# Performance work log

Hardware: AMD Instinct MI355X
Metric: run time of the kernel (lower is better)

## Reference

```python
import jax, jax.numpy as jnp
import numpy as np

B = 256        # number of graphs
NPG = 256      # nodes per graph
N = B * NPG    # total nodes
F = 128        # node feature dim
DEG = 16       # avg degree
E = N * DEG    # total edges
LAT = [32, 32, 32, 1]
D = sum(LAT)   # total_latent_dim = 97
K = 30         # sortpool k
C1, C2, KW2 = 16, 32, 5
DENSE = ((K - 2) // 2 + 1 - KW2 + 1) * C2  # 352
OUT = 2


def setup_inputs() -> dict:
    key = jax.random.key(0)
    ks = jax.random.split(key, 16)
    node_feat = jax.random.normal(ks[0], (N, F), jnp.float32)
    # edges constrained within each graph (block-diagonal adjacency)
    base = ((jnp.arange(E, dtype=jnp.int32) // (E // B)) * NPG).astype(jnp.int32)
    src = jax.random.randint(ks[1], (E,), 0, NPG, dtype=jnp.int32) + base
    dst = jax.random.randint(ks[2], (E,), 0, NPG, dtype=jnp.int32) + base
    degs = jnp.zeros((N,), jnp.int32).at[dst].add(1)  # in-degree per node
    s = 0.1
    dims = [F] + LAT
    inp = {"node_feat": node_feat, "src": src, "dst": dst, "degs": degs}
    for i in range(4):
        inp[f"W{i}"] = jax.random.normal(ks[3 + i], (dims[i], dims[i + 1]), jnp.float32) * s
        inp[f"b{i}"] = jnp.zeros((dims[i + 1],), jnp.float32)
    inp["conv1_w"] = jax.random.normal(ks[8], (C1, 1, D), jnp.float32) * s
    inp["conv1_b"] = jnp.zeros((C1,), jnp.float32)
    inp["conv2_w"] = jax.random.normal(ks[9], (C2, C1, KW2), jnp.float32) * s
    inp["conv2_b"] = jnp.zeros((C2,), jnp.float32)
    inp["out_w"] = jax.random.normal(ks[10], (DENSE, OUT), jnp.float32) * s
    inp["out_b"] = jnp.zeros((OUT,), jnp.float32)
    return inp


def reference(node_feat, W0, b0, W1, b1, W2, b2, W3, b3,
              conv1_w, conv1_b, conv2_w, conv2_b, out_w, out_b,
              src, dst, degs):
    n = node_feat.shape[0]
    deg1 = (degs.astype(node_feat.dtype) + 1.0)[:, None]  # node_degs = deg + 1
    h = node_feat
    feats = []
    for W, b in ((W0, b0), (W1, b1), (W2, b2), (W3, b3)):
        # gnn_spmm(n2n, h) + h : sparse adjacency matmul via segment add
        pooled = jnp.zeros((n, h.shape[1]), h.dtype).at[dst].add(h[src]) + h
        h = jnp.tanh((pooled @ W + b) / deg1)
        feats.append(h)
    Z = jnp.concatenate(feats, axis=1)          # [N, D]
    Zb = Z.reshape(B, NPG, D)                   # equal-sized graphs
    # sortpooling: top-k on last latent channel per graph, gather rows
    _, idx = jax.lax.top_k(Zb[:, :, -1], K)     # [B, K]
    sp = jnp.take_along_axis(Zb, idx[:, :, None], axis=1)  # [B, K, D]
    x = sp.reshape(B, 1, K * D)
    dn = ('NCH', 'OIH', 'NCH')
    x = jax.lax.conv_general_dilated(x, conv1_w, (D,), 'VALID', dimension_numbers=dn)
    x = jax.nn.relu(x + conv1_b[None, :, None])          # [B, C1, K]
    x = x.reshape(B, C1, K // 2, 2).max(axis=-1)         # maxpool1d(2,2) -> [B, C1, 15]
    x = jax.lax.conv_general_dilated(x, conv2_w, (1,), 'VALID', dimension_numbers=dn)
    x = jax.nn.relu(x + conv2_b[None, :, None])          # [B, C2, 11]
    to_dense = x.reshape(B, -1)                          # [B, 352]
    out = jax.nn.relu(to_dense @ out_w + out_b)
    return jax.nn.relu(out)  # original applies conv1d_activation twice at the end
```

## Files before the change

kernel.cpp:

```cpp
#include <hip/hip_runtime.h>

#define NPG  256
#define EPG  4096
#define FDIM 128
#define KTOP 30

__global__ __launch_bounds__(256, 1)
void dgcnn_fused(const float* __restrict__ node_feat,
                 const int* __restrict__ srcv, const int* __restrict__ dstv,
                 const int* __restrict__ degs,
                 const float* __restrict__ W0, const float* __restrict__ b0,
                 const float* __restrict__ W1, const float* __restrict__ b1,
                 const float* __restrict__ W2, const float* __restrict__ b2,
                 const float* __restrict__ W3, const float* __restrict__ b3,
                 const float* __restrict__ cw1, const float* __restrict__ cb1,
                 const float* __restrict__ cw2, const float* __restrict__ cb2,
                 const float* __restrict__ ow,  const float* __restrict__ ob,
                 float* __restrict__ outp)
{
    __shared__ float Ybuf[NPG * 33];
    __shared__ int   srclist[EPG];
    __shared__ int   offs[NPG];
    __shared__ int   cnt [NPG];
    __shared__ int   degl[NPG];
    __shared__ float invd[NPG];
    __shared__ float keys[NPG];
    __shared__ int   sel [KTOP + 2];

    const int g = blockIdx.x;
    const int t = threadIdx.x;

    int dn = degs[g * NPG + t];
    degl[t] = dn;
    cnt[t]  = 0;
    invd[t] = 1.0f / (float)(dn + 1);
    offs[t] = dn;
    __syncthreads();
    for (int s = 1; s < NPG; s <<= 1) {
        int v = (t >= s) ? offs[t - s] : 0;
        __syncthreads();
        offs[t] += v;
        __syncthreads();
    }
    int excl = offs[t] - dn;
    __syncthreads();
    offs[t] = excl;
    __syncthreads();
    {
        const int* sg = srcv + g * EPG;
        const int* dg = dstv + g * EPG;
        for (int i = 0; i < EPG / NPG; i++) {
            int e  = t + i * NPG;
            int ss = sg[e] & (NPG - 1);
            int dd = dg[e] & (NPG - 1);
            int p  = atomicAdd(&cnt[dd], 1);
            srclist[offs[dd] + p] = ss;
        }
    }

    float acc[32];
    #pragma unroll
    for (int c = 0; c < 32; c++) acc[c] = 0.f;
    {
        const float* nf = node_feat + (size_t)g * NPG * FDIM;
        for (int kc = 0; kc < 4; kc++) {
            __syncthreads();
            #pragma unroll
            for (int i = 0; i < 8; i++) {
                int Fi = t + i * 256;
                int n  = Fi >> 3, k4 = Fi & 7;
                const float4 v = *(const float4*)(nf + n * FDIM + kc * 32 + k4 * 4);
                float* p = &Ybuf[n * 33 + k4 * 4];
                p[0] = v.x; p[1] = v.y; p[2] = v.z; p[3] = v.w;
            }
            __syncthreads();
            #pragma unroll
            for (int k = 0; k < 32; k++) {
                float h = Ybuf[t * 33 + k];
                const float* wr = W0 + (kc * 32 + k) * 32;
                #pragma unroll
                for (int c = 0; c < 32; c++) acc[c] = fmaf(h, wr[c], acc[c]);
            }
        }
        __syncthreads();
        #pragma unroll
        for (int c = 0; c < 32; c++) Ybuf[t * 33 + c] = acc[c];
        __syncthreads();
    }

    float h1[32], h2[32], h3[32];
    const float iv = invd[t];
    const int   o  = offs[t];
    const int   d  = degl[t];

    auto agg = [&](float (&h)[32]) {
        #pragma unroll
        for (int c = 0; c < 32; c++) h[c] = Ybuf[t * 33 + c];
        for (int j = 0; j < d; j++) {
            int a = srclist[o + j];
            const float* yr = &Ybuf[a * 33];
            #pragma unroll
            for (int c = 0; c < 32; c++) h[c] += yr[c];
        }
    };
    auto act = [&](float (&h)[32], const float* bb) {
        #pragma unroll
        for (int c = 0; c < 32; c++) h[c] = tanhf((h[c] + bb[c]) * iv);
    };
    auto matml = [&](const float (&h)[32], const float* Wn) {
        float a[32];
        #pragma unroll
        for (int c = 0; c < 32; c++) a[c] = 0.f;
        #pragma unroll
        for (int k = 0; k < 32; k++) {
            const float* wr = Wn + k * 32;
            float hk = h[k];
            #pragma unroll
            for (int c = 0; c < 32; c++) a[c] = fmaf(hk, wr[c], a[c]);
        }
        __syncthreads();
        #pragma unroll
        for (int c = 0; c < 32; c++) Ybuf[t * 33 + c] = a[c];
        __syncthreads();
    };

    agg(h1); act(h1, b0); matml(h1, W1);
    agg(h2); act(h2, b1); matml(h2, W2);
    agg(h3); act(h3, b2);
    {
        float a3 = 0.f;
        #pragma unroll
        for (int k = 0; k < 32; k++) a3 = fmaf(h3[k], W3[k], a3);
        __syncthreads();
        Ybuf[t * 33] = a3;
        __syncthreads();
    }
    float kv;
    {
        float s = Ybuf[t * 33];
        for (int j = 0; j < d; j++) s += Ybuf[srclist[o + j] * 33];
        kv = tanhf((s + b3[0]) * iv);
        keys[t] = kv;
    }
    __syncthreads();

    int rank = 0;
    #pragma unroll 4
    for (int j = 0; j < NPG; j++) {
        float vj = keys[j];
        rank += ((vj > kv) || ((vj == kv) && (j < t))) ? 1 : 0;
    }
    if (rank < KTOP) sel[rank] = t;
    __syncthreads();

    float* sp    = (float*)srclist;
    float* x1    = sp + 30 * 97;
    float* xp    = x1 + 480;
    float* dense = xp + 240;

    if (rank < KTOP) {
        float* dp = sp + rank * 97;
        #pragma unroll
        for (int c = 0; c < 32; c++) dp[c]      = h1[c];
        #pragma unroll
        for (int c = 0; c < 32; c++) dp[32 + c] = h2[c];
        #pragma unroll
        for (int c = 0; c < 32; c++) dp[64 + c] = h3[c];
        dp[96] = kv;
    }
    __syncthreads();

    for (int idx = t; idx < 480; idx += 256) {
        int k = idx >> 4, c = idx & 15;
        float s = cb1[c];
        for (int dd = 0; dd < 97; dd++) s = fmaf(sp[k * 97 + dd], cw1[c * 97 + dd], s);
        x1[c * 30 + k] = fmaxf(s, 0.f);
    }
    __syncthreads();
    for (int idx = t; idx < 240; idx += 256) {
        int c = idx / 15, k = idx - c * 15;
        xp[idx] = fmaxf(x1[c * 30 + 2 * k], x1[c * 30 + 2 * k + 1]);
    }
    __syncthreads();
    for (int idx = t; idx < 352; idx += 256) {
        int c = idx / 11, j = idx - c * 11;
        float s = cb2[c];
        for (int i2 = 0; i2 < 16; i2++) {
            #pragma unroll
            for (int tt = 0; tt < 5; tt++)
                s = fmaf(xp[i2 * 15 + j + tt], cw2[(c * 16 + i2) * 5 + tt], s);
        }
        dense[idx] = fmaxf(s, 0.f);
    }
    __syncthreads();
    if (t < 64) {
        float a0 = 0.f, a1 = 0.f;
        for (int dd = t; dd < 352; dd += 64) {
            float v = dense[dd];
            a0 = fmaf(v, ow[dd * 2],     a0);
            a1 = fmaf(v, ow[dd * 2 + 1], a1);
        }
        #pragma unroll
        for (int off2 = 32; off2 > 0; off2 >>= 1) {
            a0 += __shfl_down(a0, off2);
            a1 += __shfl_down(a1, off2);
        }
        if (t == 0) {
            outp[g * 2 + 0] = fmaxf(a0 + ob[0], 0.f);
            outp[g * 2 + 1] = fmaxf(a1 + ob[1], 0.f);
        }
    }
}

extern "C" void kernel_launch(void* const* d_in, const int* in_sizes, int n_in,
                              void* d_out, int out_size, void* d_ws, size_t ws_size,
                              hipStream_t stream) {
    const float* node_feat = (const float*)d_in[0];
    const int*   src       = (const int*)  d_in[1];
    const int*   dst       = (const int*)  d_in[2];
    const int*   degsp     = (const int*)  d_in[3];
    const float* W0 = (const float*)d_in[4];
    const float* b0 = (const float*)d_in[5];
    const float* W1 = (const float*)d_in[6];
    const float* b1 = (const float*)d_in[7];
    const float* W2 = (const float*)d_in[8];
    const float* b2 = (const float*)d_in[9];
    const float* W3 = (const float*)d_in[10];
    const float* b3 = (const float*)d_in[11];
    const float* cw1 = (const float*)d_in[12];
    const float* cb1 = (const float*)d_in[13];
    const float* cw2 = (const float*)d_in[14];
    const float* cb2 = (const float*)d_in[15];
    const float* ow  = (const float*)d_in[16];
    const float* ob  = (const float*)d_in[17];

    dgcnn_fused<<<dim3(256), dim3(256), 0, stream>>>(
        node_feat, src, dst, degsp,
        W0, b0, W1, b1, W2, b2, W3, b3,
        cw1, cb1, cw2, cb2, ow, ob, (float*)d_out);
}
```

Baseline: 185.1 us.

## Split each node's channels across four thread groups with 1024-thread blocks

Blocks grow from 256 to 1024 threads, and each node's 32 channels are split across four thread quarters of 8 channels each. The edge source list is stored as 16-bit indices and read with vectorized int4 loads. Each layer now aggregates neighbours first and then runs the matmul on the pooled features through shared memory. The goal is to cut per-thread register pressure and serial work and raise latency hiding. The cost is extra barriers, and the last-layer aggregation still runs on only 256 threads.

```diff
diff --git a/kernel.cpp b/kernel.cpp
--- a/kernel.cpp
+++ b/kernel.cpp
@@ -4,8 +4,9 @@
 #define EPG  4096
 #define FDIM 128
 #define KTOP 30
-
-__global__ __launch_bounds__(256, 1)
+#define NT   1024
+
+__global__ __launch_bounds__(NT)
 void dgcnn_fused(const float* __restrict__ node_feat,
                  const int* __restrict__ srcv, const int* __restrict__ dstv,
                  const int* __restrict__ degs,
@@ -18,179 +19,209 @@
                  const float* __restrict__ ow,  const float* __restrict__ ob,
                  float* __restrict__ outp)
 {
-    __shared__ float Ybuf[NPG * 33];
-    __shared__ int   srclist[EPG];
+    __shared__ float Buf[NPG * 33];
+    __shared__ unsigned short srclist[EPG];
     __shared__ int   offs[NPG];
     __shared__ int   cnt [NPG];
     __shared__ int   degl[NPG];
     __shared__ float invd[NPG];
     __shared__ float keys[NPG];
-    __shared__ int   sel [KTOP + 2];
-
-    const int g = blockIdx.x;
-    const int t = threadIdx.x;
-
-    int dn = degs[g * NPG + t];
-    degl[t] = dn;
-    cnt[t]  = 0;
-    invd[t] = 1.0f / (float)(dn + 1);
-    offs[t] = dn;
+    __shared__ float sbuf[NPG];
+
+    const int g  = blockIdx.x;
+    const int t  = threadIdx.x;
+    const int n  = t & (NPG - 1);
+    const int q  = t >> 8;
+    const int c0 = q * 8;
+
+    if (t < NPG) {
+        int dn = degs[g * NPG + t];
+        degl[t] = dn;
+        cnt[t]  = 0;
+        invd[t] = 1.0f / (float)(dn + 1);
+        offs[t] = dn;
+    }
     __syncthreads();
     for (int s = 1; s < NPG; s <<= 1) {
-        int v = (t >= s) ? offs[t - s] : 0;
-        __syncthreads();
-        offs[t] += v;
-        __syncthreads();
-    }
-    int excl = offs[t] - dn;
-    __syncthreads();
-    offs[t] = excl;
-    __syncthreads();
+        int v = 0;
+        if (t < NPG && t >= s) v = offs[t - s];
+        __syncthreads();
+        if (t < NPG) offs[t] += v;
+        __syncthreads();
+    }
+    if (t < NPG) offs[t] -= degl[t];
+    __syncthreads();
+
     {
-        const int* sg = srcv + g * EPG;
-        const int* dg = dstv + g * EPG;
-        for (int i = 0; i < EPG / NPG; i++) {
-            int e  = t + i * NPG;
-            int ss = sg[e] & (NPG - 1);
-            int dd = dg[e] & (NPG - 1);
-            int p  = atomicAdd(&cnt[dd], 1);
-            srclist[offs[dd] + p] = ss;
-        }
-    }
-
-    float acc[32];
-    #pragma unroll
-    for (int c = 0; c < 32; c++) acc[c] = 0.f;
+        const int4* sg4 = (const int4*)(srcv + g * EPG);
+        const int4* dg4 = (const int4*)(dstv + g * EPG);
+        int4 s4 = sg4[t];
+        int4 d4 = dg4[t];
+        int ss[4] = {s4.x, s4.y, s4.z, s4.w};
+        int dd[4] = {d4.x, d4.y, d4.z, d4.w};
+        #pragma unroll
+        for (int i = 0; i < 4; i++) {
+            int sl = ss[i] & (NPG - 1);
+            int dl = dd[i] & (NPG - 1);
+            int p  = atomicAdd(&cnt[dl], 1);
+            srclist[offs[dl] + p] = (unsigned short)sl;
+        }
+    }
+
+    float acc[8];
+    #pragma unroll
+    for (int c = 0; c < 8; c++) acc[c] = 0.f;
     {
         const float* nf = node_feat + (size_t)g * NPG * FDIM;
         for (int kc = 0; kc < 4; kc++) {
             __syncthreads();
             #pragma unroll
-            for (int i = 0; i < 8; i++) {
-                int Fi = t + i * 256;
-                int n  = Fi >> 3, k4 = Fi & 7;
-                const float4 v = *(const float4*)(nf + n * FDIM + kc * 32 + k4 * 4);
-                float* p = &Ybuf[n * 33 + k4 * 4];
+            for (int i = 0; i < 2; i++) {
+                int f  = t + i * NT;
+                int nn = f >> 3, k4 = f & 7;
+                float4 v = *(const float4*)(nf + nn * FDIM + kc * 32 + k4 * 4);
+                float* p = &Buf[nn * 33 + k4 * 4];
                 p[0] = v.x; p[1] = v.y; p[2] = v.z; p[3] = v.w;
             }
             __syncthreads();
+            const float* wbase = W0 + (kc * 32) * 32 + c0;
             #pragma unroll
             for (int k = 0; k < 32; k++) {
-                float h = Ybuf[t * 33 + k];
-                const float* wr = W0 + (kc * 32 + k) * 32;
+                float hk = Buf[n * 33 + k];
+                const float* wr = wbase + k * 32;
                 #pragma unroll
-                for (int c = 0; c < 32; c++) acc[c] = fmaf(h, wr[c], acc[c]);
+                for (int c = 0; c < 8; c++) acc[c] = fmaf(hk, wr[c], acc[c]);
             }
         }
-        __syncthreads();
-        #pragma unroll
-        for (int c = 0; c < 32; c++) Ybuf[t * 33 + c] = acc[c];
-        __syncthreads();
-    }
-
-    float h1[32], h2[32], h3[32];
-    const float iv = invd[t];
-    const int   o  = offs[t];
-    const int   d  = degl[t];
-
-    auto agg = [&](float (&h)[32]) {
-        #pragma unroll
-        for (int c = 0; c < 32; c++) h[c] = Ybuf[t * 33 + c];
-        for (int j = 0; j < d; j++) {
-            int a = srclist[o + j];
-            const float* yr = &Ybuf[a * 33];
-            #pragma unroll
-            for (int c = 0; c < 32; c++) h[c] += yr[c];
+    }
+    __syncthreads();
+    #pragma unroll
+    for (int c = 0; c < 8; c++) Buf[n * 33 + c0 + c] = acc[c];
+    __syncthreads();
+
+    const int   o  = offs[n];
+    const int   d  = degl[n];
+    const float iv = invd[n];
+
+    auto gather8 = [&](float (&dst8)[8]) {
+        #pragma unroll
+        for (int c = 0; c < 8; c++) dst8[c] = Buf[n * 33 + c0 + c];
+        int j = 0;
+        for (; j + 3 < d; j += 4) {
+            int a0 = srclist[o + j],     a1 = srclist[o + j + 1];
+            int a2 = srclist[o + j + 2], a3 = srclist[o + j + 3];
+            const float* r0 = &Buf[a0 * 33 + c0];
+            const float* r1 = &Buf[a1 * 33 + c0];
+            const float* r2 = &Buf[a2 * 33 + c0];
+            const float* r3 = &Buf[a3 * 33 + c0];
+            #pragma unroll
+            for (int c = 0; c < 8; c++) dst8[c] += (r0[c] + r1[c]) + (r2[c] + r3[c]);
+        }
+        for (; j < d; j++) {
+            const float* r = &Buf[srclist[o + j] * 33 + c0];
+            #pragma unroll
+            for (int c = 0; c < 8; c++) dst8[c] += r[c];
         }
     };
-    auto act = [&](float (&h)[32], const float* bb) {
-        #pragma unroll
-        for (int c = 0; c < 32; c++) h[c] = tanhf((h[c] + bb[c]) * iv);
+
+    float h1s[8], h2s[8], h3s[8];
+
+    gather8(h1s);
+    #pragma unroll
+    for (int c = 0; c < 8; c++) h1s[c] = tanhf((h1s[c] + b0[c0 + c]) * iv);
+    __syncthreads();
+    #pragma unroll
+    for (int c = 0; c < 8; c++) Buf[n * 33 + c0 + c] = h1s[c];
+    __syncthreads();
+
+    auto layer32 = [&](const float* Wn, const float* bb, float (&hs)[8]) {
+        float p8[8];
+        gather8(p8);
+        __syncthreads();
+        #pragma unroll
+        for (int c = 0; c < 8; c++) Buf[n * 33 + c0 + c] = p8[c];
+        __syncthreads();
+        float y[8];
+        #pragma unroll
+        for (int c = 0; c < 8; c++) y[c] = 0.f;
+        #pragma unroll
+        for (int k = 0; k < 32; k++) {
+            float pk = Buf[n * 33 + k];
+            const float* wr = Wn + k * 32 + c0;
+            #pragma unroll
+            for (int c = 0; c < 8; c++) y[c] = fmaf(pk, wr[c], y[c]);
+        }
+        #pragma unroll
+        for (int c = 0; c < 8; c++) hs[c] = tanhf((y[c] + bb[c0 + c]) * iv);
+        __syncthreads();
+        #pragma unroll
+        for (int c = 0; c < 8; c++) Buf[n * 33 + c0 + c] = hs[c];
+        __syncthreads();
     };
-    auto matml = [&](const float (&h)[32], const float* Wn) {
-        float a[32];
-        #pragma unroll
-        for (int c = 0; c < 32; c++) a[c] = 0.f;
-        #pragma unroll
-        for (int k = 0; k < 32; k++) {
-            const float* wr = Wn + k * 32;
-            float hk = h[k];
-            #pragma unroll
-            for (int c = 0; c < 32; c++) a[c] = fmaf(hk, wr[c], a[c]);
-        }
-        __syncthreads();
-        #pragma unroll
-        for (int c = 0; c < 32; c++) Ybuf[t * 33 + c] = a[c];
-        __syncthreads();
-    };
-
-    agg(h1); act(h1, b0); matml(h1, W1);
-    agg(h2); act(h2, b1); matml(h2, W2);
-    agg(h3); act(h3, b2);
-    {
-        float a3 = 0.f;
-        #pragma unroll
-        for (int k = 0; k < 32; k++) a3 = fmaf(h3[k], W3[k], a3);
-        __syncthreads();
-        Ybuf[t * 33] = a3;
-        __syncthreads();
-    }
-    float kv;
-    {
-        float s = Ybuf[t * 33];
-        for (int j = 0; j < d; j++) s += Ybuf[srclist[o + j] * 33];
-        kv = tanhf((s + b3[0]) * iv);
-        keys[t] = kv;
-    }
-    __syncthreads();
-
+    layer32(W1, b1, h2s);
+    layer32(W2, b2, h3s);
+
+    if (t < NPG) {
+        float s = 0.f;
+        #pragma unroll
+        for (int k = 0; k < 32; k++) s = fmaf(Buf[t * 33 + k], W3[k], s);
+        sbuf[t] = s;
+    }
+    __syncthreads();
+    if (t < NPG) {
+        float s = sbuf[t];
+        int oo = offs[t], d2 = degl[t];
+        for (int j = 0; j < d2; j++) s += sbuf[srclist[oo + j]];
+        keys[t] = tanhf((s + b3[0]) * invd[t]);
+    }
+    __syncthreads();
+
+    float kv = keys[n];
     int rank = 0;
     #pragma unroll 4
     for (int j = 0; j < NPG; j++) {
         float vj = keys[j];
-        rank += ((vj > kv) || ((vj == kv) && (j < t))) ? 1 : 0;
-    }
-    if (rank < KTOP) sel[rank] = t;
-    __syncthreads();
-
-    float* sp    = (float*)srclist;
-    float* x1    = sp + 30 * 97;
+        rank += ((vj > kv) || ((vj == kv) && (j < n))) ? 1 : 0;
+    }
+
+    float* sp    = Buf;
+    float* x1    = Buf + 2910;
     float* xp    = x1 + 480;
     float* dense = xp + 240;
 
     if (rank < KTOP) {
         float* dp = sp + rank * 97;
         #pragma unroll
-        for (int c = 0; c < 32; c++) dp[c]      = h1[c];
-        #pragma unroll
-        for (int c = 0; c < 32; c++) dp[32 + c] = h2[c];
-        #pragma unroll
-        for (int c = 0; c < 32; c++) dp[64 + c] = h3[c];
-        dp[96] = kv;
-    }
-    __syncthreads();
-
-    for (int idx = t; idx < 480; idx += 256) {
-        int k = idx >> 4, c = idx & 15;
+        for (int c = 0; c < 8; c++) {
+            dp[c0 + c]      = h1s[c];
+            dp[32 + c0 + c] = h2s[c];
+            dp[64 + c0 + c] = h3s[c];
+        }
+        if (q == 0) dp[96] = kv;
+    }
+    __syncthreads();
+
+    if (t < 480) {
+        int k = t >> 4, c = t & 15;
         float s = cb1[c];
         for (int dd = 0; dd < 97; dd++) s = fmaf(sp[k * 97 + dd], cw1[c * 97 + dd], s);
         x1[c * 30 + k] = fmaxf(s, 0.f);
     }
     __syncthreads();
-    for (int idx = t; idx < 240; idx += 256) {
-        int c = idx / 15, k = idx - c * 15;
-        xp[idx] = fmaxf(x1[c * 30 + 2 * k], x1[c * 30 + 2 * k + 1]);
-    }
-    __syncthreads();
-    for (int idx = t; idx < 352; idx += 256) {
-        int c = idx / 11, j = idx - c * 11;
+    if (t < 240) {
+        int c = t / 15, k = t - c * 15;
+        xp[t] = fmaxf(x1[c * 30 + 2 * k], x1[c * 30 + 2 * k + 1]);
+    }
+    __syncthreads();
+    if (t < 352) {
+        int c = t / 11, j = t - c * 11;
         float s = cb2[c];
         for (int i2 = 0; i2 < 16; i2++) {
             #pragma unroll
             for (int tt = 0; tt < 5; tt++)
                 s = fmaf(xp[i2 * 15 + j + tt], cw2[(c * 16 + i2) * 5 + tt], s);
         }
-        dense[idx] = fmaxf(s, 0.f);
+        dense[t] = fmaxf(s, 0.f);
     }
     __syncthreads();
     if (t < 64) {
@@ -234,7 +265,7 @@
     const float* ow  = (const float*)d_in[16];
     const float* ob  = (const float*)d_in[17];
 
-    dgcnn_fused<<<dim3(256), dim3(256), 0, stream>>>(
+    dgcnn_fused<<<dim3(256), dim3(NT), 0, stream>>>(
         node_feat, src, dst, degsp,
         W0, b0, W1, b1, W2, b2, W3, b3,
         cw1, cb1, cw2, cb2, ow, ob, (float*)d_out);
```

Result: slower. 464.3 us (+150.8%).
